# Kernel tuning notes

Hardware: AMD Instinct MI355X
Metric: run time of the kernel (lower is better)

## Reference

```python
import jax, jax.numpy as jnp
import numpy as np

GAUSS_START = 0.5
GAUSS_END = 5.0
N_GAUSS = 16
N_ATOMS = 3072
N_GRAPHS = 64
K_GRID = 4096


def setup_inputs() -> dict:
    key = jax.random.key(0)
    k1, k2, k3, k4 = jax.random.split(key, 4)
    coeff = jax.random.normal(k1, (N_ATOMS, N_GAUSS), dtype=jnp.float32)
    atom_coord = jax.random.normal(k2, (N_ATOMS, 3), dtype=jnp.float32)
    grid = jax.random.normal(k3, (N_GRAPHS, K_GRID, 3), dtype=jnp.float32)
    batch = jnp.sort(jax.random.randint(k4, (N_ATOMS,), 0, N_GRAPHS, dtype=jnp.int64))
    return {"coeff": coeff, "atom_coord": atom_coord, "grid": grid, "batch": batch}


def reference(coeff, atom_coord, grid, batch):
    # Precomputed gaussian widths (buffers in the torch module)
    sigma = jnp.linspace(GAUSS_START, GAUSS_END, N_GAUSS, dtype=jnp.float32)
    sigma_r = 1.0 / (sigma * np.float32(np.sqrt(2.0 * np.pi))) ** 3  # (n_gauss,)
    sigma_2r = 1.0 / sigma ** 2  # (n_gauss,)

    # Gather per-atom grid: (N, K, 3)
    sample_vec = grid[batch] - atom_coord[:, None, :]
    r2 = jnp.sum(sample_vec ** 2, axis=-1)  # (N, K)
    # Gaussian basis on grid: (N, K, n_gauss)
    orbital = jnp.exp(-r2[..., None] * sigma_2r) * sigma_r
    # Weighted sum over gaussians: (N, K)
    density = jnp.einsum('nkg,ng->nk', orbital, coeff)
    # Scatter-add atoms back to their graph: (G, K)
    return jax.ops.segment_sum(density, batch, num_segments=N_GRAPHS)
```

## Files before the change

kernel.cpp:

```cpp
#include <hip/hip_runtime.h>
#include <cmath>

constexpr int N_GAUSS = 16;
constexpr int N_GRAPHS = 64;
constexpr int K_GRID = 4096;

constexpr int NSEG = 512;
constexpr int TSTRIDE = 528;
constexpr float RMAX = 12.0f;

constexpr int KCHUNK = 256;
constexpr int KPER = 8;
constexpr int KSPAN = KCHUNK * KPER;
constexpr int CHUNKS = K_GRID / KSPAN;
constexpr int APB = 12;

struct GaussParams {
    float ns2[N_GAUSS];
    float b[N_GAUSS];
};

__device__ __forceinline__ float fast_exp2(float x) {
    return __builtin_amdgcn_exp2f(x);
}

__global__ __launch_bounds__(256) void zero_out_kernel(float4* __restrict__ out4) {
    out4[blockIdx.x * 256 + threadIdx.x] = make_float4(0.f, 0.f, 0.f, 0.f);
}

__global__ __launch_bounds__(KCHUNK) void GaussianOrbital_kernel(
    const float* __restrict__ coeff,
    const float* __restrict__ atom_coord,
    const float* __restrict__ grid,
    const int* __restrict__ batch,
    float* __restrict__ out,
    GaussParams p, int n_atoms)
{
    __shared__ float lds[APB * TSTRIDE];

    const int chunk = blockIdx.x;
    const int ablk  = blockIdx.y;
    const int t = (int)threadIdx.x;

    const int lo = ablk * APB;
    int hi = lo + APB; if (hi > n_atoms) hi = n_atoms;

    for (int a = lo; a < hi; ++a) {
        const float* __restrict__ cf = coeff + a * N_GAUSS;
        float* __restrict__ T = lds + (a - lo) * TSTRIDE;
        for (int e = t; e <= NSEG; e += KCHUNK) {
            const float r = (float)e * (RMAX / (float)NSEG);
            const float r2 = r * r;
            float a0 = 0.f, a1 = 0.f, a2 = 0.f, a3 = 0.f;
            #pragma unroll
            for (int g = 0; g < N_GAUSS; g += 4) {
                a0 = fmaf(cf[g + 0], fast_exp2(fmaf(r2, p.ns2[g + 0], p.b[g + 0])), a0);
                a1 = fmaf(cf[g + 1], fast_exp2(fmaf(r2, p.ns2[g + 1], p.b[g + 1])), a1);
                a2 = fmaf(cf[g + 2], fast_exp2(fmaf(r2, p.ns2[g + 2], p.b[g + 2])), a2);
                a3 = fmaf(cf[g + 3], fast_exp2(fmaf(r2, p.ns2[g + 3], p.b[g + 3])), a3);
            }
            T[e] = (a0 + a1) + (a2 + a3);
        }
    }
    __syncthreads();

    int cur_g = __builtin_amdgcn_readfirstlane(batch[lo]);

    float kx[KPER], ky[KPER], kz[KPER], acc[KPER];
    auto load_grid = [&](int g) {
        #pragma unroll
        for (int j = 0; j < KPER; ++j) {
            const int k = chunk * KSPAN + j * KCHUNK + t;
            const int b = (g * K_GRID + k) * 3;
            kx[j] = grid[b + 0]; ky[j] = grid[b + 1]; kz[j] = grid[b + 2];
        }
    };
    auto flush = [&](int g) {
        #pragma unroll
        for (int j = 0; j < KPER; ++j) {
            const int k = chunk * KSPAN + j * KCHUNK + t;
            atomicAdd(&out[g * K_GRID + k], acc[j]);
            acc[j] = 0.f;
        }
    };
    load_grid(cur_g);
    #pragma unroll
    for (int j = 0; j < KPER; ++j) acc[j] = 0.f;

    for (int a = lo; a < hi; ++a) {
        const int g = __builtin_amdgcn_readfirstlane(batch[a]);
        if (g != cur_g) {
            flush(cur_g);
            cur_g = g;
            load_grid(cur_g);
        }

        const float ax = atom_coord[a * 3 + 0];
        const float ay = atom_coord[a * 3 + 1];
        const float az = atom_coord[a * 3 + 2];
        const float* __restrict__ T = lds + (a - lo) * TSTRIDE;

        float fr[KPER]; int ii[KPER];
        #pragma unroll
        for (int j = 0; j < KPER; ++j) {
            const float dx = kx[j] - ax, dy = ky[j] - ay, dz = kz[j] - az;
            const float r2 = fmaf(dx, dx, fmaf(dy, dy, dz * dz));
            float tt = __builtin_amdgcn_sqrtf(r2) * ((float)NSEG / RMAX);
            tt = fminf(tt, (float)(NSEG - 1));
            const int i = (int)tt;
            fr[j] = tt - (float)i;
            ii[j] = i;
        }
        float f0[KPER], f1[KPER];
        #pragma unroll
        for (int j = 0; j < KPER; ++j) { f0[j] = T[ii[j]]; f1[j] = T[ii[j] + 1]; }
        #pragma unroll
        for (int j = 0; j < KPER; ++j) acc[j] = acc[j] + fmaf(fr[j], f1[j] - f0[j], f0[j]);
    }

    flush(cur_g);
}

extern "C" void kernel_launch(void* const* d_in, const int* in_sizes, int n_in,
                              void* d_out, int out_size, void* d_ws, size_t ws_size,
                              hipStream_t stream)
{
    const float* coeff      = (const float*)d_in[0];
    const float* atom_coord = (const float*)d_in[1];
    const float* grid       = (const float*)d_in[2];
    const int*   batch      = (const int*)d_in[3];
    float* out = (float*)d_out;
    const int n_atoms = in_sizes[0] / N_GAUSS;

    GaussParams p;
    const double sqrt2pi = 2.50662827463100050242;
    for (int g = 0; g < N_GAUSS; ++g) {
        const double sigma = 0.5 + (5.0 - 0.5) * (double)g / (double)(N_GAUSS - 1);
        p.ns2[g] = (float)(-1.44269504088896340736 / (sigma * sigma));
        const double sr = 1.0 / (sigma * sqrt2pi * sigma * sqrt2pi * sigma * sqrt2pi);
        p.b[g] = (float)(std::log2(sr));
    }

    {
        const int nvec4 = (N_GRAPHS * K_GRID) / 4;
        hipLaunchKernelGGL(zero_out_kernel, dim3(nvec4 / 256), dim3(256), 0, stream,
                           (float4*)out);
    }
    {
        const int n_ablk = (n_atoms + APB - 1) / APB;
        dim3 gDim(CHUNKS, n_ablk);
        hipLaunchKernelGGL(GaussianOrbital_kernel, gDim, dim3(KCHUNK), 0, stream,
                           coeff, atom_coord, grid, batch, out, p, n_atoms);
    }
}
```

Before: 82.92 us.

## Build shared radial tables once via cooperative grid sync, fuse zeroing

Replaces the per-block redundant radial-table construction with one global build pass, where each block builds tables for a few atoms into workspace memory. A cooperative grid sync follows, and each block then copies its atoms' tables into LDS. Zeroing of the output is folded into the same kernel, removing a separate launch, and KPER is halved to double the number of k-chunks. The goal is to remove the redundant exp2 work repeated across chunks. In exchange it adds a grid-wide barrier and a global round trip for the tables, and needs all 1024 blocks to be co-resident for the cooperative launch.

```diff
diff --git a/kernel.cpp b/kernel.cpp
--- a/kernel.cpp
+++ b/kernel.cpp
@@ -1,5 +1,8 @@
 #include <hip/hip_runtime.h>
+#include <hip/hip_cooperative_groups.h>
 #include <cmath>
+
+namespace cg = cooperative_groups;
 
 constexpr int N_GAUSS = 16;
 constexpr int N_GRAPHS = 64;
@@ -10,10 +13,12 @@
 constexpr float RMAX = 12.0f;
 
 constexpr int KCHUNK = 256;
-constexpr int KPER = 8;
+constexpr int KPER = 4;
 constexpr int KSPAN = KCHUNK * KPER;
 constexpr int CHUNKS = K_GRID / KSPAN;
 constexpr int APB = 12;
+constexpr int NBLK = CHUNKS * 256;
+constexpr int BUILD_APB = 3;
 
 struct GaussParams {
     float ns2[N_GAUSS];
@@ -24,43 +29,58 @@
     return __builtin_amdgcn_exp2f(x);
 }
 
-__global__ __launch_bounds__(256) void zero_out_kernel(float4* __restrict__ out4) {
-    out4[blockIdx.x * 256 + threadIdx.x] = make_float4(0.f, 0.f, 0.f, 0.f);
-}
-
 __global__ __launch_bounds__(KCHUNK) void GaussianOrbital_kernel(
     const float* __restrict__ coeff,
     const float* __restrict__ atom_coord,
     const float* __restrict__ grid,
     const int* __restrict__ batch,
     float* __restrict__ out,
+    float* __restrict__ table,
     GaussParams p, int n_atoms)
 {
     __shared__ float lds[APB * TSTRIDE];
 
     const int chunk = blockIdx.x;
     const int ablk  = blockIdx.y;
+    const int blin  = ablk * CHUNKS + chunk;
     const int t = (int)threadIdx.x;
+
+    {
+        const int tid = blin * KCHUNK + t;
+        if (tid < (N_GRAPHS * K_GRID) / 4) {
+            ((float4*)out)[tid] = make_float4(0.f, 0.f, 0.f, 0.f);
+        }
+        const int a0 = blin * BUILD_APB;
+        for (int a = a0; a < a0 + BUILD_APB && a < n_atoms; ++a) {
+            const float* __restrict__ cf = coeff + a * N_GAUSS;
+            float* __restrict__ T = table + (size_t)a * TSTRIDE;
+            for (int e = t; e <= NSEG; e += KCHUNK) {
+                const float r = (float)e * (RMAX / (float)NSEG);
+                const float r2 = r * r;
+                float s0 = 0.f, s1 = 0.f, s2 = 0.f, s3 = 0.f;
+                #pragma unroll
+                for (int g = 0; g < N_GAUSS; g += 4) {
+                    s0 = fmaf(cf[g + 0], fast_exp2(fmaf(r2, p.ns2[g + 0], p.b[g + 0])), s0);
+                    s1 = fmaf(cf[g + 1], fast_exp2(fmaf(r2, p.ns2[g + 1], p.b[g + 1])), s1);
+                    s2 = fmaf(cf[g + 2], fast_exp2(fmaf(r2, p.ns2[g + 2], p.b[g + 2])), s2);
+                    s3 = fmaf(cf[g + 3], fast_exp2(fmaf(r2, p.ns2[g + 3], p.b[g + 3])), s3);
+                }
+                T[e] = (s0 + s1) + (s2 + s3);
+            }
+        }
+    }
+
+    cg::this_grid().sync();
 
     const int lo = ablk * APB;
     int hi = lo + APB; if (hi > n_atoms) hi = n_atoms;
 
-    for (int a = lo; a < hi; ++a) {
-        const float* __restrict__ cf = coeff + a * N_GAUSS;
-        float* __restrict__ T = lds + (a - lo) * TSTRIDE;
-        for (int e = t; e <= NSEG; e += KCHUNK) {
-            const float r = (float)e * (RMAX / (float)NSEG);
-            const float r2 = r * r;
-            float a0 = 0.f, a1 = 0.f, a2 = 0.f, a3 = 0.f;
-            #pragma unroll
-            for (int g = 0; g < N_GAUSS; g += 4) {
-                a0 = fmaf(cf[g + 0], fast_exp2(fmaf(r2, p.ns2[g + 0], p.b[g + 0])), a0);
-                a1 = fmaf(cf[g + 1], fast_exp2(fmaf(r2, p.ns2[g + 1], p.b[g + 1])), a1);
-                a2 = fmaf(cf[g + 2], fast_exp2(fmaf(r2, p.ns2[g + 2], p.b[g + 2])), a2);
-                a3 = fmaf(cf[g + 3], fast_exp2(fmaf(r2, p.ns2[g + 3], p.b[g + 3])), a3);
-            }
-            T[e] = (a0 + a1) + (a2 + a3);
-        }
+    {
+        const float4* __restrict__ src = (const float4*)(table + (size_t)lo * TSTRIDE);
+        float4* dst = (float4*)lds;
+        const int nvec = (hi - lo) * TSTRIDE / 4;
+        #pragma unroll 2
+        for (int i = t; i < nvec; i += KCHUNK) dst[i] = src[i];
     }
     __syncthreads();
 
@@ -129,8 +149,9 @@
     const float* atom_coord = (const float*)d_in[1];
     const float* grid       = (const float*)d_in[2];
     const int*   batch      = (const int*)d_in[3];
-    float* out = (float*)d_out;
-    const int n_atoms = in_sizes[0] / N_GAUSS;
+    float* out   = (float*)d_out;
+    float* table = (float*)d_ws;
+    int n_atoms = in_sizes[0] / N_GAUSS;
 
     GaussParams p;
     const double sqrt2pi = 2.50662827463100050242;
@@ -141,15 +162,12 @@
         p.b[g] = (float)(std::log2(sr));
     }
 
-    {
-        const int nvec4 = (N_GRAPHS * K_GRID) / 4;
-        hipLaunchKernelGGL(zero_out_kernel, dim3(nvec4 / 256), dim3(256), 0, stream,
-                           (float4*)out);
-    }
-    {
-        const int n_ablk = (n_atoms + APB - 1) / APB;
-        dim3 gDim(CHUNKS, n_ablk);
-        hipLaunchKernelGGL(GaussianOrbital_kernel, gDim, dim3(KCHUNK), 0, stream,
-                           coeff, atom_coord, grid, batch, out, p, n_atoms);
-    }
+    void* args[] = {
+        (void*)&coeff, (void*)&atom_coord, (void*)&grid, (void*)&batch,
+        (void*)&out, (void*)&table, (void*)&p, (void*)&n_atoms
+    };
+    dim3 gDim(CHUNKS, 256);
+    dim3 bDim(KCHUNK);
+    hipLaunchCooperativeKernel((void*)GaussianOrbital_kernel, gDim, bDim,
+                               args, 0, stream);
 }
```

Measured after the change: 158.9 us. +91.7%, slower.
